# Kernel optimization log

Hardware: AMD Instinct MI355X
Metric: run time of the kernel (lower is better)

Reference implementation:

```python
import jax, jax.numpy as jnp
import numpy as np

N, DEG = 20000, 16
E = N * DEG
D_IN, D_HID, D_OUT, L = 1024, 512, 128, 3


def setup_inputs() -> dict:
    key = jax.random.key(0)
    ks = jax.random.split(key, 16)
    scale = 0.02
    X = jax.random.normal(ks[0], (N, D_IN), dtype=jnp.float32)
    senders = jax.random.randint(ks[1], (E,), 0, N)
    receivers = jnp.repeat(jnp.arange(N), DEG)  # sorted, every node has DEG neighbors
    inp = {"X": X, "senders": senders, "receivers": receivers}
    ki = 2
    for l in range(L):
        din = D_IN >> l
        dh = D_HID >> l
        inp[f"lw{l}"] = jax.random.normal(ks[ki], (2 * din, dh), jnp.float32) * scale; ki += 1
        inp[f"lb{l}"] = jnp.zeros((dh,), jnp.float32)
        inp[f"aw{l}"] = jax.random.normal(ks[ki], (din, dh), jnp.float32) * scale; ki += 1
        inp[f"aq{l}"] = jax.random.normal(ks[ki], (dh,), jnp.float32) * scale; ki += 1
    inp["ow"] = jax.random.normal(ks[ki], (D_HID >> (L - 1), D_OUT), jnp.float32) * scale
    inp["ob"] = jnp.zeros((D_OUT,), jnp.float32)
    return inp


def _attend(h, senders, receivers, aw, aq):
    # scores depend only on the neighbor (sender) embedding: q @ relu(W h_j)
    logits = jnp.einsum('nh,h->n', jax.nn.relu(h @ aw), aq)            # [N]
    el = logits[senders]                                               # [E]
    m = jax.ops.segment_max(el, receivers, num_segments=N)            # per-receiver max
    w = jnp.exp(el - m[receivers])                                     # [E]
    denom = jax.ops.segment_sum(w, receivers, num_segments=N)         # [N]
    msg = jax.ops.segment_sum(w[:, None] * h[senders], receivers, num_segments=N)  # [N,D]
    return msg / denom[:, None]


def reference(X, senders, receivers,
              lw0, lb0, aw0, aq0,
              lw1, lb1, aw1, aq1,
              lw2, lb2, aw2, aq2,
              ow, ob):
    params = [(lw0, lb0, aw0, aq0), (lw1, lb1, aw1, aq1), (lw2, lb2, aw2, aq2)]
    h = X
    for lw, lb, aw, aq in params:
        hN = _attend(h, senders, receivers, aw, aq)
        h = jax.nn.relu(jnp.concatenate([h, hN], axis=1) @ lw + lb)
    return h[14] @ ow + ob
```

## Files before the change

### kernel.cpp

```cpp
#include <hip/hip_runtime.h>
#include <math.h>

typedef unsigned short ushort_t;
typedef __attribute__((ext_vector_type(8))) short short8;
typedef __attribute__((ext_vector_type(4))) float f32x4;

#define NN    20000
#define DEG   16
constexpr int MAXL2 = 1 + DEG;
constexpr int MAXL1 = MAXL2 + MAXL2*DEG;
constexpr int MAXL0 = MAXL1*DEG;
constexpr int L0PAD = 73 * 64;
constexpr int NWBLK = 512;

__device__ __forceinline__ ushort_t f2bf(float f) {
    unsigned u = __float_as_uint(f);
    return (ushort_t)((u + 0x7FFFu + ((u >> 16) & 1u)) >> 16);
}

__global__ __launch_bounds__(256)
void k_frontier(const int* __restrict__ senders,
                int* list2, int* inv2, int* list1, int* inv1,
                int* list0, int* inv0, int* list3, int* cnts, float4* zp, int n4) {
    int t = threadIdx.x;
    if (blockIdx.x > 0) {
        int i = (blockIdx.x - 1) * 256 + t;
        if (i < n4) zp[i] = make_float4(0.f, 0.f, 0.f, 0.f);
        return;
    }
    __shared__ unsigned bm[625];
    __shared__ int cnt;
    auto clear = [&]() { for (int i = t; i < 625; i += 256) bm[i] = 0u; if (t == 0) cnt = 0; };
    auto tryadd = [&](int node, int* list, int* inv) {
        unsigned bit = 1u << (node & 31);
        unsigned old = atomicOr(&bm[node >> 5], bit);
        if (!(old & bit)) { int p = atomicAdd(&cnt, 1); list[p] = node; inv[node] = p; }
    };
    clear(); __syncthreads();
    if (t < 17) { int node = (t < 16) ? senders[14 * DEG + t] : 14; tryadd(node, list2, inv2); }
    __syncthreads();
    int c2 = cnt; if (t == 0) cnts[2] = c2;
    __syncthreads(); clear(); __syncthreads();
    for (int i = t; i < c2 * 17; i += 256) {
        int r = i / 17, k = i - 17 * r;
        int node = (k < 16) ? senders[list2[r] * DEG + k] : list2[r];
        tryadd(node, list1, inv1);
    }
    __syncthreads();
    int c1 = cnt; if (t == 0) cnts[1] = c1;
    __syncthreads(); clear(); __syncthreads();
    for (int i = t; i < c1 * 16; i += 256) {
        int r = i >> 4, k = i & 15;
        tryadd(senders[list1[r] * DEG + k], list0, inv0);
    }
    __syncthreads();
    if (t == 0) { cnts[0] = cnt; cnts[3] = 1; list3[0] = 14; }
}

__global__ __launch_bounds__(256)
void k_prep(const float* __restrict__ W, ushort_t* __restrict__ WT,
            const float* __restrict__ X, const int* __restrict__ list0,
            const int* __restrict__ cnt0, ushort_t* __restrict__ Xg) {
    int t = threadIdx.x;
    if (blockIdx.x < NWBLK) {
        __shared__ float tile[32][33];
        int b = blockIdx.x;
        int bx = b & 15, by = b >> 4;
        int i0 = t >> 3, j0 = (t & 7) * 4;
        int k = by * 32 + i0, n0 = bx * 32;
        float4 v = *(const float4*)(W + (size_t)k * 512 + n0 + j0);
        tile[i0][j0] = v.x; tile[i0][j0 + 1] = v.y; tile[i0][j0 + 2] = v.z; tile[i0][j0 + 3] = v.w;
        __syncthreads();
        int n = n0 + i0, kc = j0;
        ushort_t* p = WT + (size_t)n * 1024 + by * 32 + kc;
        p[0] = f2bf(tile[kc][i0]); p[1] = f2bf(tile[kc + 1][i0]);
        p[2] = f2bf(tile[kc + 2][i0]); p[3] = f2bf(tile[kc + 3][i0]);
    } else {
        int r = blockIdx.x - NWBLK;
        int rc = *cnt0;
        ushort_t o0 = 0, o1 = 0, o2 = 0, o3 = 0;
        if (r < rc) {
            float4 v = *(const float4*)(X + (size_t)list0[r] * 1024 + t * 4);
            o0 = f2bf(v.x); o1 = f2bf(v.y); o2 = f2bf(v.z); o3 = f2bf(v.w);
        }
        ushort_t* p = Xg + (size_t)r * 1024 + t * 4;
        p[0] = o0; p[1] = o1; p[2] = o2; p[3] = o3;
    }
}

__global__ __launch_bounds__(256)
void k_logits_mfma(const ushort_t* __restrict__ Xg,
                   const ushort_t* __restrict__ WT,
                   const float* __restrict__ aq, float* __restrict__ lgc,
                   const int* __restrict__ cnt, int K) {
    __shared__ short As[64 * 40];
    __shared__ short Bs[64 * 40];
    int rcnt = *cnt;
    int row0 = blockIdx.x * 64;
    if (row0 >= rcnt) return;
    int col0 = blockIdx.y * 64;
    int t = threadIdx.x;
    int w = t >> 6, lane = t & 63;

    int sr = t >> 2, sk = (t & 3) * 8;
    const ushort_t* ap = Xg + (size_t)(row0 + sr) * K + sk;
    const ushort_t* bp = WT + (size_t)(col0 + sr) * K + sk;

    int fm = lane & 15, fq = lane >> 4;
    const short* arow = As + (w * 16 + fm) * 40 + fq * 8;
    const short* brow = Bs + fm * 40 + fq * 8;

    f32x4 acc0 = {0.f,0.f,0.f,0.f}, acc1 = {0.f,0.f,0.f,0.f};
    f32x4 acc2 = {0.f,0.f,0.f,0.f}, acc3 = {0.f,0.f,0.f,0.f};

    short8 pa = *(const short8*)(ap);
    short8 pb = *(const short8*)(bp);
    for (int k0 = 0; k0 < K; k0 += 32) {
        *(short8*)(As + sr * 40 + sk) = pa;
        *(short8*)(Bs + sr * 40 + sk) = pb;
        __syncthreads();
        if (k0 + 32 < K) {
            pa = *(const short8*)(ap + k0 + 32);
            pb = *(const short8*)(bp + k0 + 32);
        }
        short8 af = *(const short8*)arow;
        short8 b0 = *(const short8*)(brow);
        short8 b1 = *(const short8*)(brow + 16 * 40);
        short8 b2 = *(const short8*)(brow + 32 * 40);
        short8 b3 = *(const short8*)(brow + 48 * 40);
        acc0 = __builtin_amdgcn_mfma_f32_16x16x32_bf16(af, b0, acc0, 0, 0, 0);
        acc1 = __builtin_amdgcn_mfma_f32_16x16x32_bf16(af, b1, acc1, 0, 0, 0);
        acc2 = __builtin_amdgcn_mfma_f32_16x16x32_bf16(af, b2, acc2, 0, 0, 0);
        acc3 = __builtin_amdgcn_mfma_f32_16x16x32_bf16(af, b3, acc3, 0, 0, 0);
        __syncthreads();
    }

    float aqv0 = aq[col0 + fm], aqv1 = aq[col0 + 16 + fm];
    float aqv2 = aq[col0 + 32 + fm], aqv3 = aq[col0 + 48 + fm];
#pragma unroll
    for (int r = 0; r < 4; r++) {
        float v = fmaxf(acc0[r], 0.f) * aqv0 + fmaxf(acc1[r], 0.f) * aqv1
                + fmaxf(acc2[r], 0.f) * aqv2 + fmaxf(acc3[r], 0.f) * aqv3;
#pragma unroll
        for (int off = 1; off < 16; off <<= 1) v += __shfl_xor(v, off);
        if (fm == 0) atomicAdd(&lgc[row0 + w * 16 + fq * 4 + r], v);
    }
}

__global__ __launch_bounds__(256)
void k_matmul(const float* __restrict__ A1, const float* __restrict__ A2,
              const int* __restrict__ list, const int* __restrict__ inv,
              const float* __restrict__ B, const float* __restrict__ aq,
              float* __restrict__ C, const int* __restrict__ cnt,
              int amode, int omode, int K1, int K2, int NC, int KS) {
    __shared__ float As[32][68];
    __shared__ float Bs[32][64];
    __shared__ float rowsum[64];

    int rcnt = *cnt;
    int row0 = blockIdx.x * 64;
    if (row0 >= rcnt) return;
    int col0 = blockIdx.y * 64;
    int K = K1 + K2;
    int kbeg = blockIdx.z * KS;
    int kend = kbeg + KS; if (kend > K) kend = K;

    int t = threadIdx.x;
    int ty = t >> 4, tx = t & 15;
    int lr = t >> 2, kaoff = (t & 3) * 4;
    int grow = row0 + lr;
    bool rowValid = grow < rcnt;
    const float* rp1 = A1;
    const float* rp2 = A2;
    if (rowValid) {
        int hrow;
        if (amode == 0) hrow = grow;
        else { int node = list[grow]; hrow = (amode == 2) ? inv[node] : node; }
        rp1 = A1 + (size_t)hrow * K1;
        rp2 = A2 + (size_t)grow * K2;
    }
    const float* Bp = B + col0;
    int bidx0 = t, bidx1 = t + 256;

    auto loadA = [&](int k) -> float4 {
        if (!rowValid) return make_float4(0.f, 0.f, 0.f, 0.f);
        const float* src = (k < K1) ? (rp1 + k) : (rp2 + (k - K1));
        return *(const float4*)src;
    };
    auto loadB = [&](int idx, int k0) -> float4 {
        int row = idx >> 4, c4 = (idx & 15) * 4;
        return *(const float4*)(Bp + (size_t)(k0 + row) * NC + c4);
    };

    float4 pa0 = loadA(kbeg + kaoff);
    float4 pa1 = loadA(kbeg + kaoff + 16);
    float4 pb0 = loadB(bidx0, kbeg);
    float4 pb1 = loadB(bidx1, kbeg);

    float acc[4][4] = {};
    for (int k0 = kbeg; k0 < kend; k0 += 32) {
        As[kaoff + 0][lr] = pa0.x; As[kaoff + 1][lr] = pa0.y;
        As[kaoff + 2][lr] = pa0.z; As[kaoff + 3][lr] = pa0.w;
        As[kaoff + 16][lr] = pa1.x; As[kaoff + 17][lr] = pa1.y;
        As[kaoff + 18][lr] = pa1.z; As[kaoff + 19][lr] = pa1.w;
        *(float4*)&Bs[bidx0 >> 4][(bidx0 & 15) * 4] = pb0;
        *(float4*)&Bs[bidx1 >> 4][(bidx1 & 15) * 4] = pb1;
        __syncthreads();
        if (k0 + 32 < kend) {
            pa0 = loadA(k0 + 32 + kaoff);
            pa1 = loadA(k0 + 32 + kaoff + 16);
            pb0 = loadB(bidx0, k0 + 32);
            pb1 = loadB(bidx1, k0 + 32);
        }
#pragma unroll
        for (int kk = 0; kk < 32; kk++) {
            float4 a4 = *(const float4*)&As[kk][ty * 4];
            float4 b4 = *(const float4*)&Bs[kk][tx * 4];
            float a[4] = {a4.x, a4.y, a4.z, a4.w};
            float b[4] = {b4.x, b4.y, b4.z, b4.w};
#pragma unroll
            for (int i = 0; i < 4; i++)
#pragma unroll
                for (int j = 0; j < 4; j++) acc[i][j] += a[i] * b[j];
        }
        __syncthreads();
    }

    if (omode == 0) {
#pragma unroll
        for (int i = 0; i < 4; i++) {
            int r = row0 + ty * 4 + i;
            if (r < rcnt) {
                float* Crow = C + (size_t)r * NC + col0 + tx * 4;
#pragma unroll
                for (int j = 0; j < 4; j++) atomicAdd(&Crow[j], acc[i][j]);
            }
        }
    } else {
        if (t < 64) rowsum[t] = 0.f;
        __syncthreads();
        float aqv[4];
#pragma unroll
        for (int j = 0; j < 4; j++) aqv[j] = aq[col0 + tx * 4 + j];
#pragma unroll
        for (int i = 0; i < 4; i++) {
            float s = 0.f;
#pragma unroll
            for (int j = 0; j < 4; j++) {
                float v = acc[i][j];
                v = v > 0.f ? v : 0.f;
                s += v * aqv[j];
            }
            atomicAdd(&rowsum[ty * 4 + i], s);
        }
        __syncthreads();
        if (t < 64) {
            int r = row0 + t;
            if (r < rcnt) atomicAdd(&C[r], rowsum[t]);
        }
    }
}

__global__ void k_bias_relu(const float* __restrict__ C, const float* __restrict__ b,
                            float* __restrict__ H, const int* __restrict__ cnt, int ncShift) {
    int rcnt = *cnt;
    int NC = 1 << ncShift;
    int e = blockIdx.x * 256 + threadIdx.x;
    int r = e >> ncShift;
    if (r >= rcnt) return;
    int c = e & (NC - 1);
    float v = C[(size_t)r * NC + c] + b[c];
    H[(size_t)r * NC + c] = v > 0.f ? v : 0.f;
}

__global__ __launch_bounds__(256)
void k_agg(const float* __restrict__ Hsrc, const int* __restrict__ invH,
           const float* __restrict__ lgc, const int* __restrict__ invL,
           const int* __restrict__ senders,
           const int* __restrict__ listN, const int* __restrict__ cntN,
           float* __restrict__ hN, int din) {
    __shared__ int   s_row[DEG];
    __shared__ float s_w[DEG];
    __shared__ float s_scale;
    int b = blockIdx.x;
    if (b >= *cntN) return;
    int n = listN[b];
    int t = threadIdx.x;
    if (t < DEG) {
        int s = senders[n * DEG + t];
        s_row[t] = invH ? invH[s] : s;
        s_w[t] = lgc[invL ? invL[s] : s];
    }
    __syncthreads();
    if (t == 0) {
        float m = -1e30f;
        for (int k = 0; k < DEG; k++) m = fmaxf(m, s_w[k]);
        float d = 0.f;
        for (int k = 0; k < DEG; k++) { float w = expf(s_w[k] - m); s_w[k] = w; d += w; }
        s_scale = 1.f / d;
    }
    __syncthreads();
    float scale = s_scale;
    for (int dI = t; dI < din; dI += 256) {
        float acc = 0.f;
#pragma unroll
        for (int k = 0; k < DEG; k++)
            acc += s_w[k] * Hsrc[(size_t)s_row[k] * din + dI];
        hN[(size_t)b * din + dI] = acc * scale;
    }
}

__global__ __launch_bounds__(512)
void k_out(const float* __restrict__ C2, const float* __restrict__ lb2,
           const float* __restrict__ OW, const float* __restrict__ OB,
           float* __restrict__ out) {
    __shared__ float h3s[128];
    __shared__ float part[4][128];
    int t = threadIdx.x;
    if (t < 128) { float v = C2[t] + lb2[t]; h3s[t] = v > 0.f ? v : 0.f; }
    __syncthreads();
    int j = t & 127, s = t >> 7;
    float a = 0.f;
    for (int k = s * 32; k < s * 32 + 32; k++) a += h3s[k] * OW[(size_t)k * 128 + j];
    part[s][j] = a;
    __syncthreads();
    if (t < 128) out[t] = OB[t] + part[0][t] + part[1][t] + part[2][t] + part[3][t];
}

extern "C" void kernel_launch(void* const* d_in, const int* in_sizes, int n_in,
                              void* d_out, int out_size, void* d_ws, size_t ws_size,
                              hipStream_t stream) {
    const float* X       = (const float*)d_in[0];
    const int*   senders = (const int*)d_in[1];
    const float* lw0 = (const float*)d_in[3];
    const float* lb0 = (const float*)d_in[4];
    const float* aw0 = (const float*)d_in[5];
    const float* aq0 = (const float*)d_in[6];
    const float* lw1 = (const float*)d_in[7];
    const float* lb1 = (const float*)d_in[8];
    const float* aw1 = (const float*)d_in[9];
    const float* aq1 = (const float*)d_in[10];
    const float* lw2 = (const float*)d_in[11];
    const float* lb2 = (const float*)d_in[12];
    const float* aw2 = (const float*)d_in[13];
    const float* aq2 = (const float*)d_in[14];
    const float* owp = (const float*)d_in[15];
    const float* obp = (const float*)d_in[16];
    float* out = (float*)d_out;

    char* ws = (char*)d_ws;
    size_t off = 0;
    auto alloc = [&](size_t nbytes) -> void* {
        void* p = ws + off;
        off += (nbytes + 255) & ~(size_t)255;
        return p;
    };
    float* lgc0 = (float*)alloc(L0PAD * 4);
    float* lgc1 = (float*)alloc(MAXL1 * 4);
    float* lgc2 = (float*)alloc(MAXL2 * 4);
    float* C0   = (float*)alloc((size_t)MAXL1 * 512 * 4);
    float* C1   = (float*)alloc((size_t)MAXL2 * 256 * 4);
    float* C2   = (float*)alloc(128 * 4);
    size_t zero_end = off;
    int* inv0  = (int*)alloc(NN * 4);
    int* inv1  = (int*)alloc(NN * 4);
    int* inv2  = (int*)alloc(NN * 4);
    int* list0 = (int*)alloc(L0PAD * 4);
    int* list1 = (int*)alloc(MAXL1 * 4);
    int* list2 = (int*)alloc(MAXL2 * 4);
    int* list3 = (int*)alloc(4);
    int* cnts  = (int*)alloc(4 * 4);
    ushort_t* Xg  = (ushort_t*)alloc((size_t)L0PAD * 1024 * 2);
    ushort_t* awT = (ushort_t*)alloc((size_t)512 * 1024 * 2);
    float* hN0c = (float*)alloc((size_t)MAXL1 * 1024 * 4);
    float* h1c  = (float*)alloc((size_t)MAXL1 * 512 * 4);
    float* hN1c = (float*)alloc((size_t)MAXL2 * 512 * 4);
    float* h2c  = (float*)alloc((size_t)MAXL2 * 256 * 4);
    float* hN2c = (float*)alloc(256 * 4);
    (void)in_sizes; (void)n_in; (void)out_size; (void)ws_size;

    int nz4 = (int)(zero_end / 16);
    int nzb = (nz4 + 255) / 256;

    hipLaunchKernelGGL(k_frontier, dim3(1 + nzb), dim3(256), 0, stream,
                       senders, list2, inv2, list1, inv1, list0, inv0, list3, cnts,
                       (float4*)ws, nz4);
    hipLaunchKernelGGL(k_prep, dim3(NWBLK + L0PAD), dim3(256), 0, stream,
                       aw0, awT, X, list0, cnts + 0, Xg);

    hipLaunchKernelGGL(k_logits_mfma, dim3(73, 512 / 64, 1), dim3(256), 0, stream,
                       Xg, awT, aq0, lgc0, cnts + 0, 1024);
    hipLaunchKernelGGL(k_agg, dim3(MAXL1), dim3(256), 0, stream,
                       X, (const int*)nullptr, lgc0, inv0, senders, list1, cnts + 1, hN0c, 1024);
    hipLaunchKernelGGL(k_matmul, dim3((MAXL1 + 63) / 64, 512 / 64, 8), dim3(256), 0, stream,
                       X, hN0c, list1, (int*)nullptr, lw0, aq0, C0, cnts + 1,
                       1, 0, 1024, 1024, 512, 256);
    hipLaunchKernelGGL(k_bias_relu, dim3((MAXL1 * 512 + 255) / 256), dim3(256), 0, stream,
                       C0, lb0, h1c, cnts + 1, 9);

    hipLaunchKernelGGL(k_matmul, dim3((MAXL1 + 63) / 64, 256 / 64, 1), dim3(256), 0, stream,
                       h1c, h1c, list1, (int*)nullptr, aw1, aq1, lgc1, cnts + 1,
                       0, 1, 512, 0, 256, 512);
    hipLaunchKernelGGL(k_agg, dim3(MAXL2), dim3(256), 0, stream,
                       h1c, inv1, lgc1, inv1, senders, list2, cnts + 2, hN1c, 512);
    hipLaunchKernelGGL(k_matmul, dim3(1, 256 / 64, 8), dim3(256), 0, stream,
                       h1c, hN1c, list2, inv1, lw1, aq1, C1, cnts + 2,
                       2, 0, 512, 512, 256, 128);
    hipLaunchKernelGGL(k_bias_relu, dim3((MAXL2 * 256 + 255) / 256), dim3(256), 0, stream,
                       C1, lb1, h2c, cnts + 2, 8);

    hipLaunchKernelGGL(k_matmul, dim3(1, 128 / 64, 1), dim3(256), 0, stream,
                       h2c, h2c, list2, (int*)nullptr, aw2, aq2, lgc2, cnts + 2,
                       0, 1, 256, 0, 128, 256);
    hipLaunchKernelGGL(k_agg, dim3(1), dim3(256), 0, stream,
                       h2c, inv2, lgc2, inv2, senders, list3, cnts + 3, hN2c, 256);
    hipLaunchKernelGGL(k_matmul, dim3(1, 128 / 64, 4), dim3(256), 0, stream,
                       h2c, hN2c, list3, inv2, lw2, aq2, C2, cnts + 3,
                       2, 0, 256, 256, 128, 128);
    hipLaunchKernelGGL(k_out, dim3(1), dim3(512), 0, stream, C2, lb2, owp, obp, out);
}
```

Measured before the change: 281.1 us.

## Fuse all layer kernels into one persistent megakernel with grid barriers

Replaces the chain of about fourteen separate launches (frontier, prep, logits, aggregation, matmuls, bias-relu, output) with one persistent kernel of 256 blocks that separates phases with a software grid barrier. Layer-0 gathering now works directly on the list1×16 edge slots instead of a deduplicated frontier, and the weights for later layers are prefetched into cache during the first phase. The final layer and output head are computed by a single block. The aim is to remove launch gaps and intermediate round trips, at the cost of spin-barrier overhead and a grid that must be fully co-resident to avoid deadlock.

```diff
diff --git a/kernel.cpp b/kernel.cpp
--- a/kernel.cpp
+++ b/kernel.cpp
@@ -7,415 +7,545 @@
 
 #define NN    20000
 #define DEG   16
-constexpr int MAXL2 = 1 + DEG;
-constexpr int MAXL1 = MAXL2 + MAXL2*DEG;
-constexpr int MAXL0 = MAXL1*DEG;
+constexpr int MAXL2 = 17;
+constexpr int MAXL1 = 289;
 constexpr int L0PAD = 73 * 64;
-constexpr int NWBLK = 512;
+constexpr int NBLK  = 256;
+constexpr int NTHR  = 512;
+
+struct MegaP {
+    const float* X; const int* senders;
+    const float* lw0; const float* lb0; const float* aw0; const float* aq0;
+    const float* lw1; const float* lb1; const float* aw1; const float* aq1;
+    const float* lw2; const float* lb2; const float* aw2; const float* aq2;
+    const float* ow; const float* ob;
+    float* out;
+    float* lgc0; float* C0;
+    float* lgc1; float* slog;
+    int* inv0; int* inv1; int* inv2;
+    int* list1; int* list2; int* cnts;
+    ushort_t* Xg; ushort_t* awT;
+    float* hN0; float* h1; float* h2;
+    float* dummy;
+    unsigned* bar;
+    int nz4;
+};
 
 __device__ __forceinline__ ushort_t f2bf(float f) {
     unsigned u = __float_as_uint(f);
     return (ushort_t)((u + 0x7FFFu + ((u >> 16) & 1u)) >> 16);
 }
 
-__global__ __launch_bounds__(256)
-void k_frontier(const int* __restrict__ senders,
-                int* list2, int* inv2, int* list1, int* inv1,
-                int* list0, int* inv0, int* list3, int* cnts, float4* zp, int n4) {
+__device__ __forceinline__ void gbar(unsigned* bar, unsigned k) {
+    __syncthreads();
+    if (threadIdx.x == 0) {
+        __threadfence();
+        if (__hip_atomic_fetch_add(&bar[0], 1u, __ATOMIC_ACQ_REL, __HIP_MEMORY_SCOPE_AGENT)
+            == (unsigned)(NBLK - 1)) {
+            __hip_atomic_store(&bar[0], 0u, __ATOMIC_RELEASE, __HIP_MEMORY_SCOPE_AGENT);
+            __hip_atomic_store(&bar[1], k,  __ATOMIC_RELEASE, __HIP_MEMORY_SCOPE_AGENT);
+        } else {
+            while (__hip_atomic_load(&bar[1], __ATOMIC_ACQUIRE, __HIP_MEMORY_SCOPE_AGENT) < k)
+                __builtin_amdgcn_s_sleep(2);
+        }
+        __threadfence();
+    }
+    __syncthreads();
+}
+
+__global__ __launch_bounds__(NTHR, 2)
+void k_mega(MegaP p) {
+    __shared__ __align__(16) char SM[107008];
     int t = threadIdx.x;
-    if (blockIdx.x > 0) {
-        int i = (blockIdx.x - 1) * 256 + t;
-        if (i < n4) zp[i] = make_float4(0.f, 0.f, 0.f, 0.f);
-        return;
-    }
-    __shared__ unsigned bm[625];
-    __shared__ int cnt;
-    auto clear = [&]() { for (int i = t; i < 625; i += 256) bm[i] = 0u; if (t == 0) cnt = 0; };
-    auto tryadd = [&](int node, int* list, int* inv) {
-        unsigned bit = 1u << (node & 31);
-        unsigned old = atomicOr(&bm[node >> 5], bit);
-        if (!(old & bit)) { int p = atomicAdd(&cnt, 1); list[p] = node; inv[node] = p; }
-    };
-    clear(); __syncthreads();
-    if (t < 17) { int node = (t < 16) ? senders[14 * DEG + t] : 14; tryadd(node, list2, inv2); }
-    __syncthreads();
-    int c2 = cnt; if (t == 0) cnts[2] = c2;
-    __syncthreads(); clear(); __syncthreads();
-    for (int i = t; i < c2 * 17; i += 256) {
-        int r = i / 17, k = i - 17 * r;
-        int node = (k < 16) ? senders[list2[r] * DEG + k] : list2[r];
-        tryadd(node, list1, inv1);
-    }
-    __syncthreads();
-    int c1 = cnt; if (t == 0) cnts[1] = c1;
-    __syncthreads(); clear(); __syncthreads();
-    for (int i = t; i < c1 * 16; i += 256) {
-        int r = i >> 4, k = i & 15;
-        tryadd(senders[list1[r] * DEG + k], list0, inv0);
-    }
-    __syncthreads();
-    if (t == 0) { cnts[0] = cnt; cnts[3] = 1; list3[0] = 14; }
-}
-
-__global__ __launch_bounds__(256)
-void k_prep(const float* __restrict__ W, ushort_t* __restrict__ WT,
-            const float* __restrict__ X, const int* __restrict__ list0,
-            const int* __restrict__ cnt0, ushort_t* __restrict__ Xg) {
-    int t = threadIdx.x;
-    if (blockIdx.x < NWBLK) {
-        __shared__ float tile[32][33];
-        int b = blockIdx.x;
-        int bx = b & 15, by = b >> 4;
-        int i0 = t >> 3, j0 = (t & 7) * 4;
-        int k = by * 32 + i0, n0 = bx * 32;
-        float4 v = *(const float4*)(W + (size_t)k * 512 + n0 + j0);
-        tile[i0][j0] = v.x; tile[i0][j0 + 1] = v.y; tile[i0][j0 + 2] = v.z; tile[i0][j0 + 3] = v.w;
-        __syncthreads();
-        int n = n0 + i0, kc = j0;
-        ushort_t* p = WT + (size_t)n * 1024 + by * 32 + kc;
-        p[0] = f2bf(tile[kc][i0]); p[1] = f2bf(tile[kc + 1][i0]);
-        p[2] = f2bf(tile[kc + 2][i0]); p[3] = f2bf(tile[kc + 3][i0]);
+    int bid = blockIdx.x;
+    int sub = t >> 8, tl = t & 255;
+
+    if (bid == 0) {
+        unsigned* bm = (unsigned*)SM;
+        int* lloc = (int*)(SM + 2560);
+        int* pcnt = (int*)(SM + 2632);
+        for (int i = t; i < 625; i += NTHR) bm[i] = 0u;
+        if (t == 0) *pcnt = 0;
+        __syncthreads();
+        if (t < 17) {
+            int node = (t < 16) ? p.senders[14 * DEG + t] : 14;
+            unsigned bit = 1u << (node & 31);
+            unsigned old = atomicOr(&bm[node >> 5], bit);
+            if (!(old & bit)) { int q = atomicAdd(pcnt, 1); p.list2[q] = node; p.inv2[node] = q; lloc[q] = node; }
+        }
+        __syncthreads();
+        int c2 = *pcnt;
+        if (t == 0) p.cnts[2] = c2;
+        __syncthreads();
+        for (int i = t; i < 625; i += NTHR) bm[i] = 0u;
+        if (t == 0) *pcnt = 0;
+        __syncthreads();
+        for (int i = t; i < c2 * 17; i += NTHR) {
+            int r = i / 17, k = i - r * 17;
+            int node = (k < 16) ? p.senders[lloc[r] * DEG + k] : lloc[r];
+            unsigned bit = 1u << (node & 31);
+            unsigned old = atomicOr(&bm[node >> 5], bit);
+            if (!(old & bit)) { int q = atomicAdd(pcnt, 1); p.list1[q] = node; p.inv1[node] = q; }
+        }
+        __syncthreads();
+        if (t == 0) { int c1 = *pcnt; p.cnts[1] = c1; p.cnts[0] = c1 * 16; }
     } else {
-        int r = blockIdx.x - NWBLK;
-        int rc = *cnt0;
-        ushort_t o0 = 0, o1 = 0, o2 = 0, o3 = 0;
-        if (r < rc) {
-            float4 v = *(const float4*)(X + (size_t)list0[r] * 1024 + t * 4);
-            o0 = f2bf(v.x); o1 = f2bf(v.y); o2 = f2bf(v.z); o3 = f2bf(v.w);
-        }
-        ushort_t* p = Xg + (size_t)r * 1024 + t * 4;
-        p[0] = o0; p[1] = o1; p[2] = o2; p[3] = o3;
-    }
-}
-
-__global__ __launch_bounds__(256)
-void k_logits_mfma(const ushort_t* __restrict__ Xg,
-                   const ushort_t* __restrict__ WT,
-                   const float* __restrict__ aq, float* __restrict__ lgc,
-                   const int* __restrict__ cnt, int K) {
-    __shared__ short As[64 * 40];
-    __shared__ short Bs[64 * 40];
-    int rcnt = *cnt;
-    int row0 = blockIdx.x * 64;
-    if (row0 >= rcnt) return;
-    int col0 = blockIdx.y * 64;
-    int t = threadIdx.x;
-    int w = t >> 6, lane = t & 63;
-
-    int sr = t >> 2, sk = (t & 3) * 8;
-    const ushort_t* ap = Xg + (size_t)(row0 + sr) * K + sk;
-    const ushort_t* bp = WT + (size_t)(col0 + sr) * K + sk;
-
-    int fm = lane & 15, fq = lane >> 4;
-    const short* arow = As + (w * 16 + fm) * 40 + fq * 8;
-    const short* brow = Bs + fm * 40 + fq * 8;
-
-    f32x4 acc0 = {0.f,0.f,0.f,0.f}, acc1 = {0.f,0.f,0.f,0.f};
-    f32x4 acc2 = {0.f,0.f,0.f,0.f}, acc3 = {0.f,0.f,0.f,0.f};
-
-    short8 pa = *(const short8*)(ap);
-    short8 pb = *(const short8*)(bp);
-    for (int k0 = 0; k0 < K; k0 += 32) {
-        *(short8*)(As + sr * 40 + sk) = pa;
-        *(short8*)(Bs + sr * 40 + sk) = pb;
-        __syncthreads();
-        if (k0 + 32 < K) {
-            pa = *(const short8*)(ap + k0 + 32);
-            pb = *(const short8*)(bp + k0 + 32);
-        }
-        short8 af = *(const short8*)arow;
-        short8 b0 = *(const short8*)(brow);
-        short8 b1 = *(const short8*)(brow + 16 * 40);
-        short8 b2 = *(const short8*)(brow + 32 * 40);
-        short8 b3 = *(const short8*)(brow + 48 * 40);
-        acc0 = __builtin_amdgcn_mfma_f32_16x16x32_bf16(af, b0, acc0, 0, 0, 0);
-        acc1 = __builtin_amdgcn_mfma_f32_16x16x32_bf16(af, b1, acc1, 0, 0, 0);
-        acc2 = __builtin_amdgcn_mfma_f32_16x16x32_bf16(af, b2, acc2, 0, 0, 0);
-        acc3 = __builtin_amdgcn_mfma_f32_16x16x32_bf16(af, b3, acc3, 0, 0, 0);
-        __syncthreads();
-    }
-
-    float aqv0 = aq[col0 + fm], aqv1 = aq[col0 + 16 + fm];
-    float aqv2 = aq[col0 + 32 + fm], aqv3 = aq[col0 + 48 + fm];
-#pragma unroll
-    for (int r = 0; r < 4; r++) {
-        float v = fmaxf(acc0[r], 0.f) * aqv0 + fmaxf(acc1[r], 0.f) * aqv1
-                + fmaxf(acc2[r], 0.f) * aqv2 + fmaxf(acc3[r], 0.f) * aqv3;
-#pragma unroll
-        for (int off = 1; off < 16; off <<= 1) v += __shfl_xor(v, off);
-        if (fm == 0) atomicAdd(&lgc[row0 + w * 16 + fq * 4 + r], v);
-    }
-}
-
-__global__ __launch_bounds__(256)
-void k_matmul(const float* __restrict__ A1, const float* __restrict__ A2,
-              const int* __restrict__ list, const int* __restrict__ inv,
-              const float* __restrict__ B, const float* __restrict__ aq,
-              float* __restrict__ C, const int* __restrict__ cnt,
-              int amode, int omode, int K1, int K2, int NC, int KS) {
-    __shared__ float As[32][68];
-    __shared__ float Bs[32][64];
-    __shared__ float rowsum[64];
-
-    int rcnt = *cnt;
-    int row0 = blockIdx.x * 64;
-    if (row0 >= rcnt) return;
-    int col0 = blockIdx.y * 64;
-    int K = K1 + K2;
-    int kbeg = blockIdx.z * KS;
-    int kend = kbeg + KS; if (kend > K) kend = K;
-
-    int t = threadIdx.x;
-    int ty = t >> 4, tx = t & 15;
-    int lr = t >> 2, kaoff = (t & 3) * 4;
-    int grow = row0 + lr;
-    bool rowValid = grow < rcnt;
-    const float* rp1 = A1;
-    const float* rp2 = A2;
-    if (rowValid) {
-        int hrow;
-        if (amode == 0) hrow = grow;
-        else { int node = list[grow]; hrow = (amode == 2) ? inv[node] : node; }
-        rp1 = A1 + (size_t)hrow * K1;
-        rp2 = A2 + (size_t)grow * K2;
-    }
-    const float* Bp = B + col0;
-    int bidx0 = t, bidx1 = t + 256;
-
-    auto loadA = [&](int k) -> float4 {
-        if (!rowValid) return make_float4(0.f, 0.f, 0.f, 0.f);
-        const float* src = (k < K1) ? (rp1 + k) : (rp2 + (k - K1));
-        return *(const float4*)src;
-    };
-    auto loadB = [&](int idx, int k0) -> float4 {
-        int row = idx >> 4, c4 = (idx & 15) * 4;
-        return *(const float4*)(Bp + (size_t)(k0 + row) * NC + c4);
-    };
-
-    float4 pa0 = loadA(kbeg + kaoff);
-    float4 pa1 = loadA(kbeg + kaoff + 16);
-    float4 pb0 = loadB(bidx0, kbeg);
-    float4 pb1 = loadB(bidx1, kbeg);
-
-    float acc[4][4] = {};
-    for (int k0 = kbeg; k0 < kend; k0 += 32) {
-        As[kaoff + 0][lr] = pa0.x; As[kaoff + 1][lr] = pa0.y;
-        As[kaoff + 2][lr] = pa0.z; As[kaoff + 3][lr] = pa0.w;
-        As[kaoff + 16][lr] = pa1.x; As[kaoff + 17][lr] = pa1.y;
-        As[kaoff + 18][lr] = pa1.z; As[kaoff + 19][lr] = pa1.w;
-        *(float4*)&Bs[bidx0 >> 4][(bidx0 & 15) * 4] = pb0;
-        *(float4*)&Bs[bidx1 >> 4][(bidx1 & 15) * 4] = pb1;
-        __syncthreads();
-        if (k0 + 32 < kend) {
-            pa0 = loadA(k0 + 32 + kaoff);
-            pa1 = loadA(k0 + 32 + kaoff + 16);
-            pb0 = loadB(bidx0, k0 + 32);
-            pb1 = loadB(bidx1, k0 + 32);
-        }
-#pragma unroll
-        for (int kk = 0; kk < 32; kk++) {
-            float4 a4 = *(const float4*)&As[kk][ty * 4];
-            float4 b4 = *(const float4*)&Bs[kk][tx * 4];
-            float a[4] = {a4.x, a4.y, a4.z, a4.w};
-            float b[4] = {b4.x, b4.y, b4.z, b4.w};
-#pragma unroll
-            for (int i = 0; i < 4; i++)
-#pragma unroll
-                for (int j = 0; j < 4; j++) acc[i][j] += a[i] * b[j];
-        }
-        __syncthreads();
-    }
-
-    if (omode == 0) {
-#pragma unroll
-        for (int i = 0; i < 4; i++) {
-            int r = row0 + ty * 4 + i;
-            if (r < rcnt) {
-                float* Crow = C + (size_t)r * NC + col0 + tx * 4;
-#pragma unroll
-                for (int j = 0; j < 4; j++) atomicAdd(&Crow[j], acc[i][j]);
-            }
-        }
-    } else {
-        if (t < 64) rowsum[t] = 0.f;
-        __syncthreads();
-        float aqv[4];
-#pragma unroll
-        for (int j = 0; j < 4; j++) aqv[j] = aq[col0 + tx * 4 + j];
-#pragma unroll
-        for (int i = 0; i < 4; i++) {
+        for (int i = (bid - 1) * NTHR + t; i < p.nz4; i += (NBLK - 1) * NTHR)
+            ((float4*)p.lgc0)[i] = make_float4(0.f, 0.f, 0.f, 0.f);
+        {
+            float (*tile)[33] = (float(*)[33])(SM + sub * 4352);
+            for (int base = (bid - 1) * 2; base < 512; base += (NBLK - 1) * 2) {
+                int tt = base + sub;
+                int bx = tt & 15, by = tt >> 4;
+                int i0 = tl >> 3, j0 = (tl & 7) * 4;
+                float4 v = *(const float4*)(p.aw0 + (size_t)(by * 32 + i0) * 512 + bx * 32 + j0);
+                tile[i0][j0] = v.x; tile[i0][j0 + 1] = v.y; tile[i0][j0 + 2] = v.z; tile[i0][j0 + 3] = v.w;
+                __syncthreads();
+                int n = bx * 32 + i0, kc = j0;
+                ushort4 o;
+                o.x = f2bf(tile[kc][i0]);     o.y = f2bf(tile[kc + 1][i0]);
+                o.z = f2bf(tile[kc + 2][i0]); o.w = f2bf(tile[kc + 3][i0]);
+                *(ushort4*)(p.awT + (size_t)n * 1024 + by * 32 + kc) = o;
+                __syncthreads();
+            }
+        }
+        for (int b = bid - 1; b < 124; b += NBLK - 1) {
+            const float4* src; int base;
+            if (b < 64)        { src = (const float4*)p.lw1; base = b * 1024; }
+            else if (b < 96)   { src = (const float4*)p.aw1; base = (b - 64) * 1024; }
+            else if (b < 104)  { src = (const float4*)p.aw2; base = (b - 96) * 1024; }
+            else if (b < 120)  { src = (const float4*)p.lw2; base = (b - 104) * 1024; }
+            else               { src = (const float4*)p.ow;  base = (b - 120) * 1024; }
             float s = 0.f;
 #pragma unroll
-            for (int j = 0; j < 4; j++) {
-                float v = acc[i][j];
-                v = v > 0.f ? v : 0.f;
-                s += v * aqv[j];
-            }
-            atomicAdd(&rowsum[ty * 4 + i], s);
-        }
-        __syncthreads();
-        if (t < 64) {
-            int r = row0 + t;
-            if (r < rcnt) atomicAdd(&C[r], rowsum[t]);
-        }
-    }
-}
-
-__global__ void k_bias_relu(const float* __restrict__ C, const float* __restrict__ b,
-                            float* __restrict__ H, const int* __restrict__ cnt, int ncShift) {
-    int rcnt = *cnt;
-    int NC = 1 << ncShift;
-    int e = blockIdx.x * 256 + threadIdx.x;
-    int r = e >> ncShift;
-    if (r >= rcnt) return;
-    int c = e & (NC - 1);
-    float v = C[(size_t)r * NC + c] + b[c];
-    H[(size_t)r * NC + c] = v > 0.f ? v : 0.f;
-}
-
-__global__ __launch_bounds__(256)
-void k_agg(const float* __restrict__ Hsrc, const int* __restrict__ invH,
-           const float* __restrict__ lgc, const int* __restrict__ invL,
-           const int* __restrict__ senders,
-           const int* __restrict__ listN, const int* __restrict__ cntN,
-           float* __restrict__ hN, int din) {
-    __shared__ int   s_row[DEG];
-    __shared__ float s_w[DEG];
-    __shared__ float s_scale;
-    int b = blockIdx.x;
-    if (b >= *cntN) return;
-    int n = listN[b];
-    int t = threadIdx.x;
-    if (t < DEG) {
-        int s = senders[n * DEG + t];
-        s_row[t] = invH ? invH[s] : s;
-        s_w[t] = lgc[invL ? invL[s] : s];
-    }
-    __syncthreads();
-    if (t == 0) {
-        float m = -1e30f;
-        for (int k = 0; k < DEG; k++) m = fmaxf(m, s_w[k]);
-        float d = 0.f;
-        for (int k = 0; k < DEG; k++) { float w = expf(s_w[k] - m); s_w[k] = w; d += w; }
-        s_scale = 1.f / d;
-    }
-    __syncthreads();
-    float scale = s_scale;
-    for (int dI = t; dI < din; dI += 256) {
-        float acc = 0.f;
-#pragma unroll
-        for (int k = 0; k < DEG; k++)
-            acc += s_w[k] * Hsrc[(size_t)s_row[k] * din + dI];
-        hN[(size_t)b * din + dI] = acc * scale;
-    }
-}
-
-__global__ __launch_bounds__(512)
-void k_out(const float* __restrict__ C2, const float* __restrict__ lb2,
-           const float* __restrict__ OW, const float* __restrict__ OB,
-           float* __restrict__ out) {
-    __shared__ float h3s[128];
-    __shared__ float part[4][128];
-    int t = threadIdx.x;
-    if (t < 128) { float v = C2[t] + lb2[t]; h3s[t] = v > 0.f ? v : 0.f; }
-    __syncthreads();
-    int j = t & 127, s = t >> 7;
-    float a = 0.f;
-    for (int k = s * 32; k < s * 32 + 32; k++) a += h3s[k] * OW[(size_t)k * 128 + j];
-    part[s][j] = a;
-    __syncthreads();
-    if (t < 128) out[t] = OB[t] + part[0][t] + part[1][t] + part[2][t] + part[3][t];
+            for (int i = 0; i < 2; i++) {
+                float4 v = src[base + i * NTHR + t];
+                s += v.x + v.y + v.z + v.w;
+            }
+            if (s == 1234.5678f) p.dummy[0] = s;
+        }
+    }
+    gbar(p.bar, 1);
+
+    {
+        int rc = p.cnts[0];
+        for (int r = bid; r < L0PAD; r += NBLK) {
+            unsigned val = 0;
+            if (r < rc) {
+                int n = p.list1[r >> 4];
+                int s = p.senders[n * DEG + (r & 15)];
+                if (t == 0) p.inv0[s] = r;
+                float2 v = *(const float2*)(p.X + (size_t)s * 1024 + t * 2);
+                val = (unsigned)f2bf(v.x) | ((unsigned)f2bf(v.y) << 16);
+            }
+            *(unsigned*)(p.Xg + (size_t)r * 1024 + t * 2) = val;
+        }
+    }
+    gbar(p.bar, 2);
+
+    {
+        short* As = (short*)SM + sub * (2 * 64 * 40);
+        short* Bs = As + 64 * 40;
+        int w = tl >> 6, lane = tl & 63;
+        int sr = tl >> 2, sk = (tl & 3) * 8;
+        int fm = lane & 15, fq = lane >> 4;
+        const short* arow = As + (w * 16 + fm) * 40 + fq * 8;
+        const short* brow = Bs + fm * 40 + fq * 8;
+        for (int base = bid * 2; base < 584; base += NBLK * 2) {
+            int tt = base + sub;
+            int bx = tt % 73, bc = tt / 73;
+            int row0 = bx * 64, col0 = bc * 64;
+            const ushort_t* ap = p.Xg  + (size_t)(row0 + sr) * 1024 + sk;
+            const ushort_t* bp = p.awT + (size_t)(col0 + sr) * 1024 + sk;
+            f32x4 acc0 = {0.f,0.f,0.f,0.f}, acc1 = {0.f,0.f,0.f,0.f};
+            f32x4 acc2 = {0.f,0.f,0.f,0.f}, acc3 = {0.f,0.f,0.f,0.f};
+            short8 pa = *(const short8*)ap;
+            short8 pb = *(const short8*)bp;
+            for (int k0 = 0; k0 < 1024; k0 += 32) {
+                *(short8*)(As + sr * 40 + sk) = pa;
+                *(short8*)(Bs + sr * 40 + sk) = pb;
+                __syncthreads();
+                if (k0 + 32 < 1024) {
+                    pa = *(const short8*)(ap + k0 + 32);
+                    pb = *(const short8*)(bp + k0 + 32);
+                }
+                short8 af = *(const short8*)arow;
+                short8 b0 = *(const short8*)(brow);
+                short8 b1 = *(const short8*)(brow + 16 * 40);
+                short8 b2 = *(const short8*)(brow + 32 * 40);
+                short8 b3 = *(const short8*)(brow + 48 * 40);
+                acc0 = __builtin_amdgcn_mfma_f32_16x16x32_bf16(af, b0, acc0, 0, 0, 0);
+                acc1 = __builtin_amdgcn_mfma_f32_16x16x32_bf16(af, b1, acc1, 0, 0, 0);
+                acc2 = __builtin_amdgcn_mfma_f32_16x16x32_bf16(af, b2, acc2, 0, 0, 0);
+                acc3 = __builtin_amdgcn_mfma_f32_16x16x32_bf16(af, b3, acc3, 0, 0, 0);
+                __syncthreads();
+            }
+            float aqv0 = p.aq0[col0 + fm],      aqv1 = p.aq0[col0 + 16 + fm];
+            float aqv2 = p.aq0[col0 + 32 + fm], aqv3 = p.aq0[col0 + 48 + fm];
+#pragma unroll
+            for (int r = 0; r < 4; r++) {
+                float v = fmaxf(acc0[r], 0.f) * aqv0 + fmaxf(acc1[r], 0.f) * aqv1
+                        + fmaxf(acc2[r], 0.f) * aqv2 + fmaxf(acc3[r], 0.f) * aqv3;
+#pragma unroll
+                for (int off = 1; off < 16; off <<= 1) v += __shfl_xor(v, off);
+                if (fm == 0) atomicAdd(&p.lgc0[row0 + w * 16 + fq * 4 + r], v);
+            }
+        }
+    }
+    gbar(p.bar, 3);
+
+    {
+        int c1 = p.cnts[1];
+        int*   s_row = (int*)SM;
+        float* s_w   = (float*)(SM + 64);
+        float* s_sc  = (float*)(SM + 128);
+        for (int b = bid; b < c1; b += NBLK) {
+            if (t < DEG) {
+                int s = p.senders[p.list1[b] * DEG + t];
+                s_row[t] = s;
+                s_w[t] = p.lgc0[p.inv0[s]];
+            }
+            __syncthreads();
+            if (t == 0) {
+                float m = -1e30f;
+                for (int k = 0; k < DEG; k++) m = fmaxf(m, s_w[k]);
+                float d = 0.f;
+                for (int k = 0; k < DEG; k++) { float w = __expf(s_w[k] - m); s_w[k] = w; d += w; }
+                s_sc[0] = 1.f / d;
+            }
+            __syncthreads();
+            float scale = s_sc[0];
+            float2 acc = make_float2(0.f, 0.f);
+#pragma unroll
+            for (int k = 0; k < DEG; k++) {
+                float w = s_w[k];
+                float2 v = *(const float2*)(p.X + (size_t)s_row[k] * 1024 + t * 2);
+                acc.x += w * v.x; acc.y += w * v.y;
+            }
+            acc.x *= scale; acc.y *= scale;
+            *(float2*)(p.hN0 + (size_t)b * 1024 + t * 2) = acc;
+            __syncthreads();
+        }
+    }
+    gbar(p.bar, 4);
+
+    {
+        int c1 = p.cnts[1];
+        float* fb = (float*)(SM) + sub * (32 * 68 + 32 * 64);
+        float (*As)[68] = (float(*)[68])fb;
+        float (*Bs)[64] = (float(*)[64])(fb + 32 * 68);
+        for (int base = bid * 2; base < 320; base += NBLK * 2) {
+            int tt = base + sub;
+            int bx = tt % 5, rest = tt / 5;
+            int by = rest & 7, bz = rest >> 3;
+            int row0 = bx * 64, col0 = by * 64;
+            int kbeg = bz * 256;
+            int ty = tl >> 4, tx = tl & 15;
+            int lr = tl >> 2, kaoff = (tl & 3) * 4;
+            int grow = row0 + lr;
+            bool rowValid = grow < c1;
+            const float* rp1 = p.X;
+            const float* rp2 = p.hN0;
+            if (rowValid) {
+                rp1 = p.X + (size_t)p.list1[grow] * 1024;
+                rp2 = p.hN0 + (size_t)grow * 1024;
+            }
+            const float* Bp = p.lw0 + col0;
+            int bidx0 = tl, bidx1 = tl + 256;
+            auto loadA = [&](int k) -> float4 {
+                if (!rowValid) return make_float4(0.f, 0.f, 0.f, 0.f);
+                const float* src = (k < 1024) ? (rp1 + k) : (rp2 + (k - 1024));
+                return *(const float4*)src;
+            };
+            auto loadB = [&](int idx, int k0) -> float4 {
+                int row = idx >> 4, c4 = (idx & 15) * 4;
+                return *(const float4*)(Bp + (size_t)(k0 + row) * 512 + c4);
+            };
+            float4 pa0 = loadA(kbeg + kaoff);
+            float4 pa1 = loadA(kbeg + kaoff + 16);
+            float4 pb0 = loadB(bidx0, kbeg);
+            float4 pb1 = loadB(bidx1, kbeg);
+            float acc[4][4] = {};
+            for (int k0 = kbeg; k0 < kbeg + 256; k0 += 32) {
+                As[kaoff + 0][lr] = pa0.x; As[kaoff + 1][lr] = pa0.y;
+                As[kaoff + 2][lr] = pa0.z; As[kaoff + 3][lr] = pa0.w;
+                As[kaoff + 16][lr] = pa1.x; As[kaoff + 17][lr] = pa1.y;
+                As[kaoff + 18][lr] = pa1.z; As[kaoff + 19][lr] = pa1.w;
+                *(float4*)&Bs[bidx0 >> 4][(bidx0 & 15) * 4] = pb0;
+                *(float4*)&Bs[bidx1 >> 4][(bidx1 & 15) * 4] = pb1;
+                __syncthreads();
+                if (k0 + 32 < kbeg + 256) {
+                    pa0 = loadA(k0 + 32 + kaoff);
+                    pa1 = loadA(k0 + 32 + kaoff + 16);
+                    pb0 = loadB(bidx0, k0 + 32);
+                    pb1 = loadB(bidx1, k0 + 32);
+                }
+#pragma unroll
+                for (int kk = 0; kk < 32; kk++) {
+                    float4 a4 = *(const float4*)&As[kk][ty * 4];
+                    float4 b4 = *(const float4*)&Bs[kk][tx * 4];
+                    float a[4] = {a4.x, a4.y, a4.z, a4.w};
+                    float b[4] = {b4.x, b4.y, b4.z, b4.w};
+#pragma unroll
+                    for (int i = 0; i < 4; i++)
+#pragma unroll
+                        for (int j = 0; j < 4; j++) acc[i][j] += a[i] * b[j];
+                }
+                __syncthreads();
+            }
+#pragma unroll
+            for (int i = 0; i < 4; i++) {
+                int r = row0 + ty * 4 + i;
+                if (r < c1) {
+                    float* Crow = p.C0 + (size_t)r * 512 + col0 + tx * 4;
+#pragma unroll
+                    for (int j = 0; j < 4; j++) atomicAdd(&Crow[j], acc[i][j]);
+                }
+            }
+        }
+    }
+    gbar(p.bar, 5);
+
+    {
+        int c1 = p.cnts[1];
+        float* sh    = (float*)SM;
+        float* part2 = sh + 512;
+        float* red   = part2 + 512;
+        for (int r = bid; r < c1; r += NBLK) {
+            float v = p.C0[(size_t)r * 512 + t] + p.lb0[t];
+            v = v > 0.f ? v : 0.f;
+            sh[t] = v;
+            p.h1[(size_t)r * 512 + t] = v;
+            __syncthreads();
+            int c = t & 255, hh = t >> 8;
+            float dot = 0.f;
+            const float* ap = p.aw1 + c;
+            for (int k = hh * 256; k < hh * 256 + 256; k += 4)
+                dot += sh[k] * ap[(size_t)k * 256] + sh[k + 1] * ap[(size_t)(k + 1) * 256]
+                     + sh[k + 2] * ap[(size_t)(k + 2) * 256] + sh[k + 3] * ap[(size_t)(k + 3) * 256];
+            part2[t] = dot;
+            __syncthreads();
+            if (t < 256) {
+                float full = part2[t] + part2[t + 256];
+                float vv = (full > 0.f ? full : 0.f) * p.aq1[t];
+#pragma unroll
+                for (int off = 1; off < 64; off <<= 1) vv += __shfl_xor(vv, off);
+                if ((t & 63) == 0) red[t >> 6] = vv;
+            }
+            __syncthreads();
+            if (t == 0) p.lgc1[r] = red[0] + red[1] + red[2] + red[3];
+            __syncthreads();
+        }
+    }
+    gbar(p.bar, 6);
+
+    if (bid < 4) {
+        int c2 = p.cnts[2];
+        float* As    = (float*)SM;
+        float* sw    = As + 17 * 1024;
+        int*   srow  = (int*)(sw + 272);
+        int*   orow  = srow + 272;
+        float* psum  = (float*)(SM + 71888);
+        for (int i = t; i < c2 * 16; i += NTHR) {
+            int j = i >> 4, k = i & 15;
+            int s = p.senders[p.list2[j] * DEG + k];
+            int rr = p.inv1[s];
+            srow[i] = rr;
+            sw[i] = p.lgc1[rr];
+        }
+        if (t < c2) orow[t] = p.inv1[p.list2[t]];
+        __syncthreads();
+        if (t < c2) {
+            float m = -1e30f;
+            for (int k = 0; k < 16; k++) m = fmaxf(m, sw[t * 16 + k]);
+            float d = 0.f;
+            for (int k = 0; k < 16; k++) { float w = __expf(sw[t * 16 + k] - m); sw[t * 16 + k] = w; d += w; }
+            float inv = 1.f / d;
+            for (int k = 0; k < 16; k++) sw[t * 16 + k] *= inv;
+        }
+        __syncthreads();
+        for (int e = t; e < c2 * 128; e += NTHR) {
+            int j = e >> 7, d4 = (e & 127) * 4;
+            *(float4*)&As[j * 1024 + d4] = *(const float4*)&p.h1[(size_t)orow[j] * 512 + d4];
+            float4 a = make_float4(0.f, 0.f, 0.f, 0.f);
+#pragma unroll
+            for (int k = 0; k < 16; k++) {
+                float w = sw[j * 16 + k];
+                float4 v = *(const float4*)&p.h1[(size_t)srow[j * 16 + k] * 512 + d4];
+                a.x += w * v.x; a.y += w * v.y; a.z += w * v.z; a.w += w * v.w;
+            }
+            *(float4*)&As[j * 1024 + 512 + d4] = a;
+        }
+        __syncthreads();
+        int c = t & 63, s = t >> 6;
+        int gc = bid * 64 + c;
+        float acc[17];
+#pragma unroll
+        for (int j = 0; j < 17; j++) acc[j] = 0.f;
+        for (int k = s * 128; k < s * 128 + 128; k += 4) {
+            float b0 = p.lw1[(size_t)(k + 0) * 256 + gc];
+            float b1 = p.lw1[(size_t)(k + 1) * 256 + gc];
+            float b2 = p.lw1[(size_t)(k + 2) * 256 + gc];
+            float b3 = p.lw1[(size_t)(k + 3) * 256 + gc];
+#pragma unroll
+            for (int j = 0; j < 17; j++) {
+                float4 a = *(const float4*)&As[j * 1024 + k];
+                acc[j] += a.x * b0 + a.y * b1 + a.z * b2 + a.w * b3;
+            }
+        }
+#pragma unroll
+        for (int j = 0; j < 17; j++) psum[s * 1088 + j * 64 + c] = acc[j];
+        __syncthreads();
+        for (int e = t; e < c2 * 64; e += NTHR) {
+            int j = e >> 6, cc = e & 63;
+            float v = 0.f;
+#pragma unroll
+            for (int s2 = 0; s2 < 8; s2++) v += psum[s2 * 1088 + j * 64 + cc];
+            v += p.lb1[bid * 64 + cc];
+            p.h2[(size_t)j * 256 + bid * 64 + cc] = v > 0.f ? v : 0.f;
+        }
+    }
+    gbar(p.bar, 7);
+
+    {
+        int c2 = p.cnts[2];
+        if (bid < c2) {
+            float* shr  = (float*)SM;
+            float* part = shr + 256;
+            float* red  = part + 512;
+            if (t < 256) shr[t] = p.h2[(size_t)bid * 256 + t];
+            __syncthreads();
+            int c = t & 127, hh = t >> 7;
+            float dot = 0.f;
+            const float* ap = p.aw2 + c;
+            for (int k = hh * 64; k < hh * 64 + 64; k++) dot += shr[k] * ap[(size_t)k * 128];
+            part[t] = dot;
+            __syncthreads();
+            if (t < 128) {
+                float full = part[t] + part[t + 128] + part[t + 256] + part[t + 384];
+                float v = (full > 0.f ? full : 0.f) * p.aq2[t];
+#pragma unroll
+                for (int off = 1; off < 64; off <<= 1) v += __shfl_xor(v, off);
+                if ((t & 63) == 0) red[t >> 6] = v;
+            }
+            __syncthreads();
+            if (t == 0) p.slog[bid] = red[0] + red[1];
+        }
+    }
+    gbar(p.bar, 8);
+
+    if (bid == 0) {
+        float* h3in  = (float*)SM;
+        float* sh3   = h3in + 512;
+        float* psumB = sh3 + 128;
+        float* swt   = psumB + 2048;
+        int*   srow2 = (int*)(swt + 16);
+        if (t < 16) srow2[t] = p.inv2[p.senders[14 * DEG + t]];
+        __syncthreads();
+        if (t == 0) {
+            float lw[16];
+            float m = -1e30f;
+            for (int k = 0; k < 16; k++) { lw[k] = p.slog[srow2[k]]; m = fmaxf(m, lw[k]); }
+            float d = 0.f;
+            for (int k = 0; k < 16; k++) { float w = __expf(lw[k] - m); swt[k] = w; d += w; }
+            float inv = 1.f / d;
+            for (int k = 0; k < 16; k++) swt[k] *= inv;
+        }
+        __syncthreads();
+        int srow14 = p.inv2[14];
+        if (t < 256) {
+            float a = 0.f;
+#pragma unroll
+            for (int k = 0; k < 16; k++) a += swt[k] * p.h2[(size_t)srow2[k] * 256 + t];
+            h3in[256 + t] = a;
+        } else {
+            int d = t - 256;
+            h3in[d] = p.h2[(size_t)srow14 * 256 + d];
+        }
+        __syncthreads();
+        {
+            int cg = t & 31, s = t >> 5;
+            float4 acc = make_float4(0.f, 0.f, 0.f, 0.f);
+            const float* bp = p.lw2 + cg * 4;
+            for (int k = s * 32; k < s * 32 + 32; k++) {
+                float4 bv = *(const float4*)(bp + (size_t)k * 128);
+                float a = h3in[k];
+                acc.x += a * bv.x; acc.y += a * bv.y; acc.z += a * bv.z; acc.w += a * bv.w;
+            }
+            *(float4*)&psumB[s * 128 + cg * 4] = acc;
+        }
+        __syncthreads();
+        if (t < 128) {
+            float v = p.lb2[t];
+#pragma unroll
+            for (int s = 0; s < 16; s++) v += psumB[s * 128 + t];
+            sh3[t] = v > 0.f ? v : 0.f;
+        }
+        __syncthreads();
+        {
+            int cg = t & 31, s = t >> 5;
+            float4 acc = make_float4(0.f, 0.f, 0.f, 0.f);
+            const float* bp = p.ow + cg * 4;
+            for (int k = s * 8; k < s * 8 + 8; k++) {
+                float4 bv = *(const float4*)(bp + (size_t)k * 128);
+                float a = sh3[k];
+                acc.x += a * bv.x; acc.y += a * bv.y; acc.z += a * bv.z; acc.w += a * bv.w;
+            }
+            *(float4*)&psumB[s * 128 + cg * 4] = acc;
+        }
+        __syncthreads();
+        if (t < 128) {
+            float v = p.ob[t];
+#pragma unroll
+            for (int s = 0; s < 16; s++) v += psumB[s * 128 + t];
+            p.out[t] = v;
+        }
+    }
 }
 
 extern "C" void kernel_launch(void* const* d_in, const int* in_sizes, int n_in,
                               void* d_out, int out_size, void* d_ws, size_t ws_size,
                               hipStream_t stream) {
-    const float* X       = (const float*)d_in[0];
-    const int*   senders = (const int*)d_in[1];
-    const float* lw0 = (const float*)d_in[3];
-    const float* lb0 = (const float*)d_in[4];
-    const float* aw0 = (const float*)d_in[5];
-    const float* aq0 = (const float*)d_in[6];
-    const float* lw1 = (const float*)d_in[7];
-    const float* lb1 = (const float*)d_in[8];
-    const float* aw1 = (const float*)d_in[9];
-    const float* aq1 = (const float*)d_in[10];
-    const float* lw2 = (const float*)d_in[11];
-    const float* lb2 = (const float*)d_in[12];
-    const float* aw2 = (const float*)d_in[13];
-    const float* aq2 = (const float*)d_in[14];
-    const float* owp = (const float*)d_in[15];
-    const float* obp = (const float*)d_in[16];
-    float* out = (float*)d_out;
+    MegaP p;
+    p.X       = (const float*)d_in[0];
+    p.senders = (const int*)d_in[1];
+    p.lw0 = (const float*)d_in[3];  p.lb0 = (const float*)d_in[4];
+    p.aw0 = (const float*)d_in[5];  p.aq0 = (const float*)d_in[6];
+    p.lw1 = (const float*)d_in[7];  p.lb1 = (const float*)d_in[8];
+    p.aw1 = (const float*)d_in[9];  p.aq1 = (const float*)d_in[10];
+    p.lw2 = (const float*)d_in[11]; p.lb2 = (const float*)d_in[12];
+    p.aw2 = (const float*)d_in[13]; p.aq2 = (const float*)d_in[14];
+    p.ow  = (const float*)d_in[15]; p.ob  = (const float*)d_in[16];
+    p.out = (float*)d_out;
 
     char* ws = (char*)d_ws;
     size_t off = 0;
     auto alloc = [&](size_t nbytes) -> void* {
-        void* p = ws + off;
+        void* q = ws + off;
         off += (nbytes + 255) & ~(size_t)255;
-        return p;
+        return q;
     };
-    float* lgc0 = (float*)alloc(L0PAD * 4);
-    float* lgc1 = (float*)alloc(MAXL1 * 4);
-    float* lgc2 = (float*)alloc(MAXL2 * 4);
-    float* C0   = (float*)alloc((size_t)MAXL1 * 512 * 4);
-    float* C1   = (float*)alloc((size_t)MAXL2 * 256 * 4);
-    float* C2   = (float*)alloc(128 * 4);
+    p.lgc0 = (float*)alloc(L0PAD * 4);
+    p.C0   = (float*)alloc((size_t)MAXL1 * 512 * 4);
     size_t zero_end = off;
-    int* inv0  = (int*)alloc(NN * 4);
-    int* inv1  = (int*)alloc(NN * 4);
-    int* inv2  = (int*)alloc(NN * 4);
-    int* list0 = (int*)alloc(L0PAD * 4);
-    int* list1 = (int*)alloc(MAXL1 * 4);
-    int* list2 = (int*)alloc(MAXL2 * 4);
-    int* list3 = (int*)alloc(4);
-    int* cnts  = (int*)alloc(4 * 4);
-    ushort_t* Xg  = (ushort_t*)alloc((size_t)L0PAD * 1024 * 2);
-    ushort_t* awT = (ushort_t*)alloc((size_t)512 * 1024 * 2);
-    float* hN0c = (float*)alloc((size_t)MAXL1 * 1024 * 4);
-    float* h1c  = (float*)alloc((size_t)MAXL1 * 512 * 4);
-    float* hN1c = (float*)alloc((size_t)MAXL2 * 512 * 4);
-    float* h2c  = (float*)alloc((size_t)MAXL2 * 256 * 4);
-    float* hN2c = (float*)alloc(256 * 4);
+    p.lgc1  = (float*)alloc(MAXL1 * 4);
+    p.slog  = (float*)alloc(MAXL2 * 4);
+    p.inv0  = (int*)alloc(NN * 4);
+    p.inv1  = (int*)alloc(NN * 4);
+    p.inv2  = (int*)alloc(NN * 4);
+    p.list1 = (int*)alloc(MAXL1 * 4);
+    p.list2 = (int*)alloc(MAXL2 * 4);
+    p.cnts  = (int*)alloc(16);
+    p.dummy = (float*)alloc(16);
+    p.bar   = (unsigned*)alloc(16);
+    p.Xg    = (ushort_t*)alloc((size_t)L0PAD * 1024 * 2);
+    p.awT   = (ushort_t*)alloc((size_t)512 * 1024 * 2);
+    p.hN0   = (float*)alloc((size_t)MAXL1 * 1024 * 4);
+    p.h1    = (float*)alloc((size_t)MAXL1 * 512 * 4);
+    p.h2    = (float*)alloc((size_t)MAXL2 * 256 * 4);
+    p.nz4   = (int)(zero_end / 16);
     (void)in_sizes; (void)n_in; (void)out_size; (void)ws_size;
 
-    int nz4 = (int)(zero_end / 16);
-    int nzb = (nz4 + 255) / 256;
-
-    hipLaunchKernelGGL(k_frontier, dim3(1 + nzb), dim3(256), 0, stream,
-                       senders, list2, inv2, list1, inv1, list0, inv0, list3, cnts,
-                       (float4*)ws, nz4);
-    hipLaunchKernelGGL(k_prep, dim3(NWBLK + L0PAD), dim3(256), 0, stream,
-                       aw0, awT, X, list0, cnts + 0, Xg);
-
-    hipLaunchKernelGGL(k_logits_mfma, dim3(73, 512 / 64, 1), dim3(256), 0, stream,
-                       Xg, awT, aq0, lgc0, cnts + 0, 1024);
-    hipLaunchKernelGGL(k_agg, dim3(MAXL1), dim3(256), 0, stream,
-                       X, (const int*)nullptr, lgc0, inv0, senders, list1, cnts + 1, hN0c, 1024);
-    hipLaunchKernelGGL(k_matmul, dim3((MAXL1 + 63) / 64, 512 / 64, 8), dim3(256), 0, stream,
-                       X, hN0c, list1, (int*)nullptr, lw0, aq0, C0, cnts + 1,
-                       1, 0, 1024, 1024, 512, 256);
-    hipLaunchKernelGGL(k_bias_relu, dim3((MAXL1 * 512 + 255) / 256), dim3(256), 0, stream,
-                       C0, lb0, h1c, cnts + 1, 9);
-
-    hipLaunchKernelGGL(k_matmul, dim3((MAXL1 + 63) / 64, 256 / 64, 1), dim3(256), 0, stream,
-                       h1c, h1c, list1, (int*)nullptr, aw1, aq1, lgc1, cnts + 1,
-                       0, 1, 512, 0, 256, 512);
-    hipLaunchKernelGGL(k_agg, dim3(MAXL2), dim3(256), 0, stream,
-                       h1c, inv1, lgc1, inv1, senders, list2, cnts + 2, hN1c, 512);
-    hipLaunchKernelGGL(k_matmul, dim3(1, 256 / 64, 8), dim3(256), 0, stream,
-                       h1c, hN1c, list2, inv1, lw1, aq1, C1, cnts + 2,
-                       2, 0, 512, 512, 256, 128);
-    hipLaunchKernelGGL(k_bias_relu, dim3((MAXL2 * 256 + 255) / 256), dim3(256), 0, stream,
-                       C1, lb1, h2c, cnts + 2, 8);
-
-    hipLaunchKernelGGL(k_matmul, dim3(1, 128 / 64, 1), dim3(256), 0, stream,
-                       h2c, h2c, list2, (int*)nullptr, aw2, aq2, lgc2, cnts + 2,
-                       0, 1, 256, 0, 128, 256);
-    hipLaunchKernelGGL(k_agg, dim3(1), dim3(256), 0, stream,
-                       h2c, inv2, lgc2, inv2, senders, list3, cnts + 3, hN2c, 256);
-    hipLaunchKernelGGL(k_matmul, dim3(1, 128 / 64, 4), dim3(256), 0, stream,
-                       h2c, hN2c, list3, inv2, lw2, aq2, C2, cnts + 3,
-                       2, 0, 256, 256, 128, 128);
-    hipLaunchKernelGGL(k_out, dim3(1), dim3(512), 0, stream, C2, lb2, owp, obp, out);
+    hipMemsetAsync(p.bar, 0, 16, stream);
+    hipLaunchKernelGGL(k_mega, dim3(NBLK), dim3(NTHR), 0, stream, p);
 }
```

After: 674.7 us. 140% more time.
